# Kernel optimization log

Hardware: AMD Instinct MI355X
Metric: run time of the kernel (lower is better)

The kernel has to match this reference:

```python
import jax, jax.numpy as jnp
import numpy as np

SEQ_LEN = 8
NUM_HEADS = 8
LN_EPS = 1e-5
GN_EPS = 64e-5  # GroupNorm eps = head_dim * 1e-5 (RWKV7 convention, head_dim=64)


def layer_norm(x, w, b):
    mu = x.mean(-1, keepdims=True)
    var = ((x - mu) ** 2).mean(-1, keepdims=True)
    return (x - mu) / jnp.sqrt(var + LN_EPS) * w + b


def token_shift(x):
    # delta = shift(x) - x; shift prepends one zero token along time
    return jnp.pad(x, ((0, 0), (1, 0), (0, 0)))[:, :-1] - x


def group_norm(x, w, b, H):
    B, T, C = x.shape
    xh = x.reshape(B, T, H, C // H)
    mu = xh.mean(-1, keepdims=True)
    var = ((xh - mu) ** 2).mean(-1, keepdims=True)
    return ((xh - mu) / jnp.sqrt(var + GN_EPS)).reshape(B, T, C) * w + b


def rwkv7_scan(r, w, k, v, a, b, H):
    # Generalized delta-rule recurrence (RWKV7):
    #   S_t = S_{t-1} * diag(exp(-exp(w_t))) + (S_{t-1} a_t) b_t^T + v_t k_t^T
    #   o_t = S_t r_t
    B, T, C = r.shape
    N = C // H

    def tm(x):  # [B,T,C] -> [T,B,H,N] (time-major for scan)
        return x.reshape(B, T, H, N).transpose(1, 0, 2, 3)

    decay = jnp.exp(-jnp.exp(tm(w)))
    rs, ks, vs, as_, bs = tm(r), tm(k), tm(v), tm(a), tm(b)

    def step(S, inp):
        rt, dt, kt, vt, at, bt = inp  # each [B,H,N]
        sa = jnp.einsum('bhij,bhj->bhi', S, at)
        S = (S * dt[:, :, None, :]
             + sa[..., None] * bt[:, :, None, :]
             + vt[..., None] * kt[:, :, None, :])
        return S, jnp.einsum('bhij,bhj->bhi', S, rt)

    S0 = jnp.zeros((B, H, N, N), r.dtype)
    _, out = jax.lax.scan(step, S0, (rs, decay, ks, vs, as_, bs))
    return out.transpose(1, 0, 2, 3).reshape(B, T, C)


def _forward(image_tensor, pos_emb, xm, w0, w1, w2, a0, a1, a2, v0, v1, v2,
             g1, g2, kkp, kap, rkp, Wr, Wk, Wv, Wo, lnx_w, lnx_b,
             ln1_w, ln1_b, ln2_w, ln2_b, fxk, Wkey, Wval, lnf_w, lnf_b):
    EB, C, ih, iw = image_tensor.shape
    B = EB // SEQ_LEN
    H = NUM_HEADS
    x = image_tensor.transpose(0, 2, 3, 1).reshape(EB, ih * iw, C)
    x = (x + pos_emb).reshape(B, SEQ_LEN * ih * iw, C)  # [B, T, C]
    L = Wr.shape[0]
    v_first = None
    for l in range(L):
        # ---- time mix (RWKV7 attention) ----
        h = layer_norm(x, ln1_w[l], ln1_b[l])
        Bh, T, _ = h.shape
        dx = token_shift(h)
        xr, xw, xk, xv, xa, xg = [h + dx * xm[l, i] for i in range(6)]
        r = xr @ Wr[l]
        w = -jax.nn.softplus(-(w0[l] + jnp.tanh(xw @ w1[l]) @ w2[l])) - 0.5
        k = xk @ Wk[l]
        v = xv @ Wv[l]
        if v_first is None:
            v_first = v
        else:
            v = v + (v_first - v) * jax.nn.sigmoid(v0[l] + (xv @ v1[l]) @ v2[l])
        a = jax.nn.sigmoid(a0[l] + (xa @ a1[l]) @ a2[l])  # in-context lr
        g = jax.nn.sigmoid(xg @ g1[l]) @ g2[l]
        kk = (k * kkp[l]).reshape(Bh, T, H, -1)
        kk = kk / jnp.maximum(jnp.linalg.norm(kk, axis=-1, keepdims=True), 1e-12)
        kk = kk.reshape(Bh, T, C)
        k = k * (1.0 + (a - 1.0) * kap[l])
        o = rwkv7_scan(r, w, k, v, -kk, kk * a, H)
        o = group_norm(o, lnx_w[l], lnx_b[l], H)
        r4, k4, v4 = (t.reshape(Bh, T, H, -1) for t in (r, k, v))
        o = o + ((r4 * k4 * rkp[l]).sum(-1, keepdims=True) * v4).reshape(Bh, T, C)
        x = x + (o * g) @ Wo[l]
        # ---- channel mix (squared-ReLU FFN) ----
        h = layer_norm(x, ln2_w[l], ln2_b[l])
        kf = h + token_shift(h) * fxk[l]
        x = x + jnp.square(jax.nn.relu(kf @ Wkey[l])) @ Wval[l]
    x = layer_norm(x, lnf_w, lnf_b)
    return x.reshape(EB, ih, iw, C).transpose(0, 3, 1, 2)


def setup_inputs() -> dict:
    key = jax.random.key(0)
    ks = jax.random.split(key, 24)
    L, C, H = 8, 512, 8
    DW, DA, DV, DG, FF = 64, 64, 32, 128, 2048
    EB, IV, IW = 32, 8, 16
    FS = IV * IW

    def n(k, shape, s=0.02):
        return jax.random.normal(k, shape, jnp.float32) * s

    return dict(
        image_tensor=jax.random.normal(ks[0], (EB, C, IV, IW), jnp.float32),
        pos_emb=n(ks[1], (1, FS, C)),
        xm=jax.random.uniform(ks[2], (L, 6, C), jnp.float32),
        w0=n(ks[3], (L, C), 0.5) - 0.5,
        w1=n(ks[4], (L, C, DW), 0.02), w2=n(ks[5], (L, DW, C), 0.1),
        a0=jnp.zeros((L, C), jnp.float32),
        a1=n(ks[6], (L, C, DA)), a2=n(ks[7], (L, DA, C), 0.1),
        v0=jnp.ones((L, C), jnp.float32),
        v1=n(ks[8], (L, C, DV)), v2=n(ks[9], (L, DV, C), 0.1),
        g1=n(ks[10], (L, C, DG)), g2=n(ks[11], (L, DG, C), 0.1),
        kkp=jnp.full((L, C), 0.85, jnp.float32),
        kap=jnp.ones((L, C), jnp.float32),
        rkp=n(ks[12], (L, H, C // H), 0.3),
        Wr=n(ks[13], (L, C, C)), Wk=n(ks[14], (L, C, C)),
        Wv=n(ks[15], (L, C, C)), Wo=n(ks[16], (L, C, C)),
        lnx_w=jnp.ones((L, C), jnp.float32), lnx_b=jnp.zeros((L, C), jnp.float32),
        ln1_w=jnp.ones((L, C), jnp.float32), ln1_b=jnp.zeros((L, C), jnp.float32),
        ln2_w=jnp.ones((L, C), jnp.float32), ln2_b=jnp.zeros((L, C), jnp.float32),
        fxk=jax.random.uniform(ks[17], (L, C), jnp.float32),
        Wkey=n(ks[18], (L, C, FF)), Wval=n(ks[19], (L, FF, C)),
        lnf_w=jnp.ones((C,), jnp.float32), lnf_b=jnp.zeros((C,), jnp.float32),
    )


def reference(image_tensor, pos_emb, xm, w0, w1, w2, a0, a1, a2, v0, v1, v2,
              g1, g2, kkp, kap, rkp, Wr, Wk, Wv, Wo, lnx_w, lnx_b,
              ln1_w, ln1_b, ln2_w, ln2_b, fxk, Wkey, Wval, lnf_w, lnf_b):
    return _forward(image_tensor, pos_emb, xm, w0, w1, w2, a0, a1, a2, v0, v1,
                    v2, g1, g2, kkp, kap, rkp, Wr, Wk, Wv, Wo, lnx_w, lnx_b,
                    ln1_w, ln1_b, ln2_w, ln2_b, fxk, Wkey, Wval, lnf_w, lnf_b)
```

## Files before the change

kernel.cpp:

```cpp
#include <hip/hip_runtime.h>
#include <hip/hip_bf16.h>
#include <math.h>


#define NTOK 4096
#define CDIM 512
#define TT   1024
#define LC   64
#define NCH  16
#define TB   8

#define BM 128
#define BK 32

enum { EPI_NONE=0, EPI_TANH, EPI_SIG, EPI_DECAY, EPI_SIGB, EPI_VMIX, EPI_RELU2, EPI_ADD };

typedef short bf16x8 __attribute__((ext_vector_type(8)));
typedef float f32x4 __attribute__((ext_vector_type(4)));
typedef unsigned short ushort_t;

__device__ __forceinline__ float wsum64(float v) {
#pragma unroll
  for (int s = 1; s < 64; s <<= 1) v += __shfl_xor(v, s);
  return v;
}
__device__ __forceinline__ float gsum8(float v) {
  v += __shfl_xor(v, 1); v += __shfl_xor(v, 2); v += __shfl_xor(v, 4);
  return v;
}
__device__ __forceinline__ float sigm(float z) { return 1.f / (1.f + expf(-z)); }
__device__ __forceinline__ ushort_t f2bf(float x) {
  return __builtin_bit_cast(unsigned short, __float2bfloat16(x));
}
__device__ __forceinline__ void glds16(const void* g, void* l) {
  __builtin_amdgcn_global_load_lds(
      (const __attribute__((address_space(1))) void*)g,
      (__attribute__((address_space(3))) void*)l, 16, 0, 0);
}

struct Seg {
  const ushort_t* A; const ushort_t* B; void* C;
  const float* bias; const float* e1;
  int N; int K; int epi; int obf;
};
struct Segs4 { Seg s[4]; };

template<int BNt>
__global__ __launch_bounds__(256) void ggemm_k(Segs4 segs) {
  const Seg sg = segs.s[blockIdx.z];
  if (sg.epi < 0) return;
  constexpr int NCHK = 8 + BNt / 16;
  constexpr int LPW  = NCHK / 4;
  constexpr int WNF  = BNt / 32;
  __shared__ ushort_t As[3][BM * BK];
  __shared__ ushort_t Bs[3][BNt * BK];
  const ushort_t* __restrict__ A = sg.A;
  const ushort_t* __restrict__ B = sg.B;
  const int N = sg.N, K = sg.K;
  const int tid = threadIdx.x;
  const int wave = tid >> 6, lane = tid & 63;
  const int m0 = blockIdx.x * BM, n0 = blockIdx.y * BNt;
  const int wm = (wave >> 1) << 6, wn = (wave & 1) * (BNt / 2);

  f32x4 zero = {0.f, 0.f, 0.f, 0.f};
  f32x4 acc[4][WNF];
#pragma unroll
  for (int i = 0; i < 4; ++i)
#pragma unroll
    for (int j = 0; j < WNF; ++j) acc[i][j] = zero;

  const int crow = lane >> 2;
  const int soff = (((lane & 3) ^ (crow & 3)) << 3);
  const ushort_t* gptr[LPW];
  ushort_t* lbase[LPW];
  int lstr[LPW];
#pragma unroll
  for (int i = 0; i < LPW; ++i) {
    const int c = wave + 4 * i;
    if (c < 8) {
      gptr[i] = A + (size_t)(m0 + c * 16 + crow) * K + soff;
      lbase[i] = &As[0][c * 512 + lane * 8];
      lstr[i] = BM * BK;
    } else {
      gptr[i] = B + (size_t)(n0 + (c - 8) * 16 + crow) * K + soff;
      lbase[i] = &Bs[0][(c - 8) * 512 + lane * 8];
      lstr[i] = BNt * BK;
    }
  }

#define STAGE(bf_, k0_)                                        \
  { _Pragma("unroll") for (int i = 0; i < LPW; ++i)            \
      glds16(gptr[i] + (k0_), lbase[i] + (bf_) * lstr[i]); }

  const int rA = wm + (lane & 15);
  const int rB = wn + (lane & 15);
  const int kb = (((lane >> 4) ^ (lane & 3)) << 3);

#define COMPUTE(bf_)                                                          \
  {                                                                           \
    bf16x8 av[4], bvv[WNF];                                                   \
    _Pragma("unroll") for (int f = 0; f < 4; ++f)                             \
      av[f] = *(const bf16x8*)(&As[bf_][(rA + f * 16) * 32 + kb]);            \
    _Pragma("unroll") for (int f = 0; f < WNF; ++f)                           \
      bvv[f] = *(const bf16x8*)(&Bs[bf_][(rB + f * 16) * 32 + kb]);           \
    _Pragma("unroll") for (int i = 0; i < 4; ++i)                             \
      _Pragma("unroll") for (int j = 0; j < WNF; ++j)                         \
        acc[i][j] = __builtin_amdgcn_mfma_f32_16x16x32_bf16(av[i], bvv[j],    \
                                                            acc[i][j], 0, 0, 0); \
  }

  const int nk = K / BK;
  STAGE(0, 0);
  if (nk > 1) STAGE(1, BK);
  int bc = 0, bs = 2;
  for (int k = 0; k + 1 < nk; ++k) {
    asm volatile("s_waitcnt vmcnt(%0)" :: "i"(LPW) : "memory");
    __builtin_amdgcn_s_barrier();
    if (k + 2 < nk) {
      STAGE(bs, (k + 2) * BK);
      bs = (bs == 2) ? 0 : bs + 1;
    }
    COMPUTE(bc);
    bc = (bc == 2) ? 0 : bc + 1;
  }
  asm volatile("s_waitcnt vmcnt(0)" ::: "memory");
  __builtin_amdgcn_s_barrier();
  COMPUTE(bc);
#undef STAGE
#undef COMPUTE

  void* Cout = sg.C;
  const float* bias = sg.bias;
  const float* e1 = sg.e1;
  const int em = m0 + wm + ((lane >> 4) << 2);
  const int en = n0 + wn + (lane & 15);

#define EPI_STORE(EPI_, OBF_)                                                 \
  { _Pragma("unroll") for (int fi = 0; fi < 4; ++fi) {                        \
      _Pragma("unroll") for (int fj = 0; fj < WNF; ++fj) {                    \
        const int gn = en + fj * 16;                                          \
        if (gn < N) {                                                         \
          _Pragma("unroll") for (int rr = 0; rr < 4; ++rr) {                  \
            const int gm = em + fi * 16 + rr;                                 \
            const size_t idx = (size_t)gm * N + gn;                           \
            const float y = acc[fi][fj][rr];                                  \
            float outv;                                                       \
            if (EPI_ == EPI_NONE) { outv = y; }                               \
            else if (EPI_ == EPI_TANH) { outv = tanhf(y); }                   \
            else if (EPI_ == EPI_SIG) { outv = sigm(y); }                     \
            else if (EPI_ == EPI_DECAY) {                                     \
              const float z = bias[gn] + y;                                   \
              const float w = -log1pf(expf(-z)) - 0.5f;                       \
              outv = expf(-expf(w));                                          \
            } else if (EPI_ == EPI_SIGB) { outv = sigm(bias[gn] + y); }       \
            else if (EPI_ == EPI_VMIX) {                                      \
              const float vr = ((float*)Cout)[idx];                           \
              outv = vr + (e1[idx] - vr) * sigm(bias[gn] + y);                \
            } else if (EPI_ == EPI_RELU2) {                                   \
              const float t = fmaxf(y, 0.f); outv = t * t;                    \
            } else { outv = ((float*)Cout)[idx] + y; }                        \
            if (OBF_) ((ushort_t*)Cout)[idx] = f2bf(outv);                    \
            else      ((float*)Cout)[idx] = outv;                             \
          }                                                                   \
        }                                                                     \
      } } }

  switch (sg.epi) {
    case EPI_NONE:  if (sg.obf) EPI_STORE(EPI_NONE, 1) else EPI_STORE(EPI_NONE, 0); break;
    case EPI_TANH:  EPI_STORE(EPI_TANH, 1); break;
    case EPI_SIG:   EPI_STORE(EPI_SIG, 1); break;
    case EPI_DECAY: EPI_STORE(EPI_DECAY, 0); break;
    case EPI_SIGB:  EPI_STORE(EPI_SIGB, 0); break;
    case EPI_VMIX:  EPI_STORE(EPI_VMIX, 0); break;
    case EPI_RELU2: EPI_STORE(EPI_RELU2, 1); break;
    case EPI_ADD:   EPI_STORE(EPI_ADD, 0); break;
  }
#undef EPI_STORE
}

__global__ __launch_bounds__(256) void wprep_k(
    const float* __restrict__ in, ushort_t* __restrict__ out,
    int K, int N, int Npad)
{
  __shared__ float t[32][33];
  const int l = blockIdx.z;
  const int n0 = blockIdx.x * 32, k0 = blockIdx.y * 32;
  const int tx = threadIdx.x & 31, ty = threadIdx.x >> 5;
  const float* src = in + (size_t)l * K * N;
  ushort_t* dst = out + (size_t)l * Npad * K;
#pragma unroll
  for (int i = 0; i < 32; i += 8) {
    const int k = k0 + ty + i, n = n0 + tx;
    t[ty + i][tx] = (n < N) ? src[(size_t)k * N + n] : 0.f;
  }
  __syncthreads();
#pragma unroll
  for (int i = 0; i < 32; i += 8) {
    const int n = n0 + ty + i, k = k0 + tx;
    dst[(size_t)n * K + k] = f2bf(t[tx][ty + i]);
  }
}

__global__ __launch_bounds__(256) void lnmix6_k(
    const float* __restrict__ x, const float* __restrict__ w,
    const float* __restrict__ b, const float* __restrict__ xml,
    ushort_t* __restrict__ xr, ushort_t* __restrict__ xw,
    ushort_t* __restrict__ xk, ushort_t* __restrict__ xv,
    ushort_t* __restrict__ xa, ushort_t* __restrict__ xg)
{
  const int m = blockIdx.x * 4 + (threadIdx.x >> 6);
  const int lane = threadIdx.x & 63;
  const int c0 = lane << 3;
  const size_t idx = (size_t)m * CDIM + c0;
  const bool first = ((m & (TT - 1)) == 0);
  float v[8], p[8];
  *(float4*)&v[0] = *(const float4*)&x[idx];
  *(float4*)&v[4] = *(const float4*)&x[idx + 4];
  if (first) {
#pragma unroll
    for (int j = 0; j < 8; ++j) p[j] = 0.f;
  } else {
    *(float4*)&p[0] = *(const float4*)&x[idx - CDIM];
    *(float4*)&p[4] = *(const float4*)&x[idx - CDIM + 4];
  }
  float s = 0.f, sp = 0.f;
#pragma unroll
  for (int j = 0; j < 8; ++j) { s += v[j]; sp += p[j]; }
  s = wsum64(s); sp = wsum64(sp);
  const float mu = s * (1.f / 512.f), mup = sp * (1.f / 512.f);
  float q = 0.f, qp = 0.f;
#pragma unroll
  for (int j = 0; j < 8; ++j) {
    const float d1 = v[j] - mu, d2 = p[j] - mup;
    q += d1 * d1; qp += d2 * d2;
  }
  q = wsum64(q); qp = wsum64(qp);
  const float is = rsqrtf(q * (1.f / 512.f) + 1e-5f);
  const float isp = rsqrtf(qp * (1.f / 512.f) + 1e-5f);
  float wc[8], bc[8];
  *(float4*)&wc[0] = *(const float4*)&w[c0]; *(float4*)&wc[4] = *(const float4*)&w[c0 + 4];
  *(float4*)&bc[0] = *(const float4*)&b[c0]; *(float4*)&bc[4] = *(const float4*)&b[c0 + 4];
  float hv[8], dx[8];
#pragma unroll
  for (int j = 0; j < 8; ++j) {
    hv[j] = (v[j] - mu) * is * wc[j] + bc[j];
    const float hp = first ? 0.f : (p[j] - mup) * isp * wc[j] + bc[j];
    dx[j] = hp - hv[j];
  }
  ushort_t* outs[6] = {xr, xw, xk, xv, xa, xg};
#pragma unroll
  for (int o = 0; o < 6; ++o) {
    float mc[8];
    *(float4*)&mc[0] = *(const float4*)&xml[o * CDIM + c0];
    *(float4*)&mc[4] = *(const float4*)&xml[o * CDIM + c0 + 4];
    bf16x8 pk;
#pragma unroll
    for (int j = 0; j < 8; ++j) pk[j] = (short)f2bf(fmaf(dx[j], mc[j], hv[j]));
    *(bf16x8*)&outs[o][idx] = pk;
  }
}

__global__ __launch_bounds__(256) void lnmix1_k(
    const float* __restrict__ x, const float* __restrict__ w,
    const float* __restrict__ b, const float* __restrict__ coef,
    ushort_t* __restrict__ kf)
{
  const int m = blockIdx.x * 4 + (threadIdx.x >> 6);
  const int lane = threadIdx.x & 63;
  const int c0 = lane << 3;
  const size_t idx = (size_t)m * CDIM + c0;
  const bool first = ((m & (TT - 1)) == 0);
  float v[8], p[8];
  *(float4*)&v[0] = *(const float4*)&x[idx];
  *(float4*)&v[4] = *(const float4*)&x[idx + 4];
  if (first) {
#pragma unroll
    for (int j = 0; j < 8; ++j) p[j] = 0.f;
  } else {
    *(float4*)&p[0] = *(const float4*)&x[idx - CDIM];
    *(float4*)&p[4] = *(const float4*)&x[idx - CDIM + 4];
  }
  float s = 0.f, sp = 0.f;
#pragma unroll
  for (int j = 0; j < 8; ++j) { s += v[j]; sp += p[j]; }
  s = wsum64(s); sp = wsum64(sp);
  const float mu = s * (1.f / 512.f), mup = sp * (1.f / 512.f);
  float q = 0.f, qp = 0.f;
#pragma unroll
  for (int j = 0; j < 8; ++j) {
    const float d1 = v[j] - mu, d2 = p[j] - mup;
    q += d1 * d1; qp += d2 * d2;
  }
  q = wsum64(q); qp = wsum64(qp);
  const float is = rsqrtf(q * (1.f / 512.f) + 1e-5f);
  const float isp = rsqrtf(qp * (1.f / 512.f) + 1e-5f);
  bf16x8 pk;
#pragma unroll
  for (int j = 0; j < 8; ++j) {
    const float wc = w[c0 + j], bc = b[c0 + j];
    const float hv = (v[j] - mu) * is * wc + bc;
    const float hp = first ? 0.f : (p[j] - mup) * isp * wc + bc;
    pk[j] = (short)f2bf(fmaf(hp - hv, coef[c0 + j], hv));
  }
  *(bf16x8*)&kf[idx] = pk;
}

__global__ __launch_bounds__(256) void prep_k(
    float* __restrict__ k, const float* __restrict__ a,
    const float* __restrict__ kkp, const float* __restrict__ kap,
    float* __restrict__ aa, float* __restrict__ bb)
{
  const int m = blockIdx.x * 4 + (threadIdx.x >> 6);
  const int lane = threadIdx.x & 63;
  const int c0 = lane << 3;
  const size_t idx = (size_t)m * CDIM + c0;
  float kv[8], av[8], kp[8], ka[8];
  *(float4*)&kv[0] = *(const float4*)&k[idx];     *(float4*)&kv[4] = *(const float4*)&k[idx + 4];
  *(float4*)&av[0] = *(const float4*)&a[idx];     *(float4*)&av[4] = *(const float4*)&a[idx + 4];
  *(float4*)&kp[0] = *(const float4*)&kkp[c0];    *(float4*)&kp[4] = *(const float4*)&kkp[c0 + 4];
  *(float4*)&ka[0] = *(const float4*)&kap[c0];    *(float4*)&ka[4] = *(const float4*)&kap[c0 + 4];
  float kk[8], ss = 0.f;
#pragma unroll
  for (int j = 0; j < 8; ++j) { kk[j] = kv[j] * kp[j]; ss += kk[j] * kk[j]; }
  ss = gsum8(ss);
  const float rden = 1.f / fmaxf(sqrtf(ss), 1e-12f);
  float oaa[8], obb[8], okk[8];
#pragma unroll
  for (int j = 0; j < 8; ++j) {
    const float kkn = kk[j] * rden;
    oaa[j] = -kkn;
    obb[j] = kkn * av[j];
    okk[j] = kv[j] * (1.f + (av[j] - 1.f) * ka[j]);
  }
  *(float4*)&aa[idx] = *(float4*)&oaa[0]; *(float4*)&aa[idx + 4] = *(float4*)&oaa[4];
  *(float4*)&bb[idx] = *(float4*)&obb[0]; *(float4*)&bb[idx + 4] = *(float4*)&obb[4];
  *(float4*)&k[idx]  = *(float4*)&okk[0]; *(float4*)&k[idx + 4]  = *(float4*)&okk[4];
}

__global__ __launch_bounds__(256) void post_k(
    const float* __restrict__ o, const float* __restrict__ r,
    const float* __restrict__ k, const float* __restrict__ v,
    const float* __restrict__ g, const float* __restrict__ gw,
    const float* __restrict__ gb, const float* __restrict__ rkp,
    ushort_t* __restrict__ og)
{
  const int m = blockIdx.x * 4 + (threadIdx.x >> 6);
  const int lane = threadIdx.x & 63;
  const int c0 = lane << 3;
  const size_t idx = (size_t)m * CDIM + c0;
  float ov[8], rv[8], kv[8], vv[8], gv[8], rp[8];
  *(float4*)&ov[0] = *(const float4*)&o[idx];   *(float4*)&ov[4] = *(const float4*)&o[idx + 4];
  *(float4*)&rv[0] = *(const float4*)&r[idx];   *(float4*)&rv[4] = *(const float4*)&r[idx + 4];
  *(float4*)&kv[0] = *(const float4*)&k[idx];   *(float4*)&kv[4] = *(const float4*)&k[idx + 4];
  *(float4*)&vv[0] = *(const float4*)&v[idx];   *(float4*)&vv[4] = *(const float4*)&v[idx + 4];
  *(float4*)&gv[0] = *(const float4*)&g[idx];   *(float4*)&gv[4] = *(const float4*)&g[idx + 4];
  *(float4*)&rp[0] = *(const float4*)&rkp[c0];  *(float4*)&rp[4] = *(const float4*)&rkp[c0 + 4];
  float s = 0.f, dot = 0.f;
#pragma unroll
  for (int j = 0; j < 8; ++j) { s += ov[j]; dot += rv[j] * kv[j] * rp[j]; }
  s = gsum8(s); dot = gsum8(dot);
  const float mu = s * (1.f / 64.f);
  float q = 0.f;
#pragma unroll
  for (int j = 0; j < 8; ++j) { const float d = ov[j] - mu; q += d * d; }
  q = gsum8(q);
  const float is = rsqrtf(q * (1.f / 64.f) + 64e-5f);
  bf16x8 pk;
#pragma unroll
  for (int j = 0; j < 8; ++j) {
    const float gn = (ov[j] - mu) * is * gw[c0 + j] + gb[c0 + j];
    pk[j] = (short)f2bf((gn + dot * vv[j]) * gv[j]);
  }
  *(bf16x8*)&og[idx] = pk;
}

__global__ __launch_bounds__(512) void ln_final_k(
    const float* __restrict__ x, const float* __restrict__ w,
    const float* __restrict__ b, float* __restrict__ out)
{
  const int m = blockIdx.x, c = threadIdx.x;
  const size_t idx = (size_t)m * CDIM + c;
  const float v = x[idx];
  __shared__ float red[8], red2[8];
  float s = wsum64(v);
  if ((c & 63) == 0) red[c >> 6] = s;
  __syncthreads();
  float tot = 0.f;
#pragma unroll
  for (int u = 0; u < 8; ++u) tot += red[u];
  const float mu = tot * (1.f / 512.f);
  const float dv = v - mu;
  float s2 = wsum64(dv * dv);
  if ((c & 63) == 0) red2[c >> 6] = s2;
  __syncthreads();
  float vt = 0.f;
#pragma unroll
  for (int u = 0; u < 8; ++u) vt += red2[u];
  const float y = dv * rsqrtf(vt * (1.f / 512.f) + 1e-5f) * w[c] + b[c];
  const int bidx = m >> 10, t = m & 1023;
  const int p = t & 127, eb = bidx * 8 + (t >> 7);
  out[((size_t)eb * CDIM + c) * 128 + p] = y;
}

__global__ __launch_bounds__(512) void build_x_k(
    const float* __restrict__ img, const float* __restrict__ pos,
    float* __restrict__ x)
{
  const int m = blockIdx.x, c = threadIdx.x;
  const int bidx = m >> 10, t = m & 1023;
  const int p = t & 127, eb = bidx * 8 + (t >> 7);
  x[(size_t)m * CDIM + c] =
      img[((size_t)eb * CDIM + c) * 128 + p] + pos[(size_t)p * CDIM + c];
}

__global__ __launch_bounds__(256) void scan1_k(
    const float* __restrict__ d, const float* __restrict__ k,
    const float* __restrict__ v, const float* __restrict__ aa,
    const float* __restrict__ bb,
    float* __restrict__ P, float* __restrict__ Q)
{
  const int ch = blockIdx.x, bh = blockIdx.y;
  const int b = bh >> 3, hh = bh & 7;
  const int tid = threadIdx.x;
  const int i = tid >> 2, j0 = (tid & 3) << 4;
  float S[16], Pr[16];
#pragma unroll
  for (int u = 0; u < 16; ++u) { S[u] = 0.f; Pr[u] = (j0 + u == i) ? 1.f : 0.f; }

  __shared__ float sbuf[3][5 * TB * 64];
  const size_t base = (size_t)b * TT * CDIM + (size_t)ch * LC * CDIM + hh * 64;
  const float* srcs[5] = {d, k, v, aa, bb};
  const int f0 = tid, f1 = tid + 256, f2 = tid + 512;
  const float* gp0 = srcs[f0 >> 7] + base + (size_t)((f0 >> 4) & 7) * CDIM + ((f0 & 15) << 2);
  const float* gp1 = srcs[f1 >> 7] + base + (size_t)((f1 >> 4) & 7) * CDIM + ((f1 & 15) << 2);
  const float* gp2 = (tid < 128)
      ? srcs[f2 >> 7] + base + (size_t)((f2 >> 4) & 7) * CDIM + ((f2 & 15) << 2)
      : srcs[0];

#define STAGE1(bf_, goff_)                                     \
  {                                                            \
    glds16(gp0 + (goff_), &sbuf[bf_][f0 << 2]);                \
    glds16(gp1 + (goff_), &sbuf[bf_][f1 << 2]);                \
    if (tid < 128) glds16(gp2 + (goff_), &sbuf[bf_][f2 << 2]); \
  }

#define CGRP1(bf_)                                                              \
  {                                                                             \
    const float* sb0 = sbuf[bf_];                                               \
    _Pragma("unroll") for (int tt = 0; tt < TB; ++tt) {                         \
      const float* sd  = sb0 + 0 * TB * 64 + tt * 64;                           \
      const float* sk  = sb0 + 1 * TB * 64 + tt * 64;                           \
      const float* sv  = sb0 + 2 * TB * 64 + tt * 64;                           \
      const float* sa  = sb0 + 3 * TB * 64 + tt * 64;                           \
      const float* sbv = sb0 + 4 * TB * 64 + tt * 64;                           \
      float ps = 0.f, pp = 0.f;                                                 \
      _Pragma("unroll") for (int jj = 0; jj < 16; ++jj) {                       \
        ps = fmaf(S[jj],  sa[j0 + jj], ps);                                     \
        pp = fmaf(Pr[jj], sa[j0 + jj], pp);                                     \
      }                                                                         \
      ps += __shfl_xor(ps, 1); ps += __shfl_xor(ps, 2);                         \
      pp += __shfl_xor(pp, 1); pp += __shfl_xor(pp, 2);                         \
      const float vi = sv[i];                                                   \
      _Pragma("unroll") for (int jj = 0; jj < 16; ++jj) {                       \
        S[jj]  = fmaf(S[jj],  sd[j0 + jj], fmaf(ps, sbv[j0 + jj], vi * sk[j0 + jj])); \
        Pr[jj] = fmaf(Pr[jj], sd[j0 + jj], pp * sbv[j0 + jj]);                  \
      }                                                                         \
    }                                                                           \
  }

  constexpr int NG = LC / TB;
  STAGE1(0, 0);
  STAGE1(1, (size_t)TB * CDIM);
  int bc = 0, bs = 2;
  for (int g = 0; g + 1 < NG; ++g) {
    if (tid < 128) { asm volatile("s_waitcnt vmcnt(3)" ::: "memory"); }
    else           { asm volatile("s_waitcnt vmcnt(2)" ::: "memory"); }
    __builtin_amdgcn_s_barrier();
    if (g + 2 < NG) {
      STAGE1(bs, (size_t)(g + 2) * TB * CDIM);
      bs = (bs == 2) ? 0 : bs + 1;
    }
    CGRP1(bc);
    bc = (bc == 2) ? 0 : bc + 1;
  }
  asm volatile("s_waitcnt vmcnt(0)" ::: "memory");
  __builtin_amdgcn_s_barrier();
  CGRP1(bc);
#undef STAGE1
#undef CGRP1

  const size_t ob = ((size_t)(bh * NCH + ch)) * 4096 + (size_t)i * 64 + j0;
#pragma unroll
  for (int u = 0; u < 4; ++u) {
    *(float4*)&Q[ob + 4 * u] = make_float4(S[4*u], S[4*u+1], S[4*u+2], S[4*u+3]);
    *(float4*)&P[ob + 4 * u] = make_float4(Pr[4*u], Pr[4*u+1], Pr[4*u+2], Pr[4*u+3]);
  }
}

__global__ __launch_bounds__(512) void scan2_k(
    const float* __restrict__ P, const float* __restrict__ Q,
    float* __restrict__ Sst)
{
  const int tid = threadIdx.x;
  const int f0 = tid << 2;
  const int r0 = tid >> 4;
  const int c0 = (tid & 15) << 2;
  __shared__ float sP[4096];
  __shared__ float sS[4096];
  float4 S0 = {0.f, 0.f, 0.f, 0.f}, S1 = {0.f, 0.f, 0.f, 0.f};
  const size_t cbase = (size_t)blockIdx.x * NCH * 4096;
  float4 pf0 = *(const float4*)&P[cbase + f0];
  float4 pf1 = *(const float4*)&P[cbase + f0 + 2048];

  for (int c = 0; c < NCH; ++c) {
    const size_t cb = cbase + (size_t)c * 4096;
    *(float4*)&Sst[cb + f0] = S0;
    *(float4*)&Sst[cb + f0 + 2048] = S1;
    __syncthreads();
    *(float4*)&sP[f0] = pf0;  *(float4*)&sP[f0 + 2048] = pf1;
    *(float4*)&sS[f0] = S0;   *(float4*)&sS[f0 + 2048] = S1;
    __syncthreads();
    if (c + 1 < NCH) {
      pf0 = *(const float4*)&P[cb + 4096 + f0];
      pf1 = *(const float4*)&P[cb + 4096 + f0 + 2048];
    }
    const float4 q0 = *(const float4*)&Q[cb + f0];
    const float4 q1 = *(const float4*)&Q[cb + f0 + 2048];

    float a00 = 0.f, a01 = 0.f, a02 = 0.f, a03 = 0.f;
    float a10 = 0.f, a11 = 0.f, a12 = 0.f, a13 = 0.f;
    const float* sS0 = &sS[r0 * 64];
    const float* sS1 = &sS[(r0 + 32) * 64];
#pragma unroll
    for (int mm = 0; mm < 64; ++mm) {
      const float4 p4 = *(const float4*)&sP[mm * 64 + c0];
      const float u0 = sS0[mm], u1 = sS1[mm];
      a00 = fmaf(u0, p4.x, a00); a01 = fmaf(u0, p4.y, a01);
      a02 = fmaf(u0, p4.z, a02); a03 = fmaf(u0, p4.w, a03);
      a10 = fmaf(u1, p4.x, a10); a11 = fmaf(u1, p4.y, a11);
      a12 = fmaf(u1, p4.z, a12); a13 = fmaf(u1, p4.w, a13);
    }
    S0.x = a00 + q0.x; S0.y = a01 + q0.y; S0.z = a02 + q0.z; S0.w = a03 + q0.w;
    S1.x = a10 + q1.x; S1.y = a11 + q1.y; S1.z = a12 + q1.z; S1.w = a13 + q1.w;
  }
}

__global__ __launch_bounds__(256) void scan3_k(
    const float* __restrict__ r, const float* __restrict__ d,
    const float* __restrict__ k, const float* __restrict__ v,
    const float* __restrict__ aa, const float* __restrict__ bb,
    const float* __restrict__ Sst, float* __restrict__ o)
{
  const int ch = blockIdx.x, bh = blockIdx.y;
  const int b = bh >> 3, hh = bh & 7;
  const int tid = threadIdx.x;
  const int i = tid >> 2, q = tid & 3, j0 = q << 4;
  float S[16];
  const size_t sb_ = ((size_t)(bh * NCH + ch)) * 4096 + (size_t)i * 64 + j0;
#pragma unroll
  for (int u = 0; u < 4; ++u) {
    const float4 s4 = *(const float4*)&Sst[sb_ + 4 * u];
    S[4*u] = s4.x; S[4*u+1] = s4.y; S[4*u+2] = s4.z; S[4*u+3] = s4.w;
  }

  __shared__ float sbuf[3][6 * TB * 64];
  const size_t base = (size_t)b * TT * CDIM + (size_t)ch * LC * CDIM + hh * 64;
  const float* srcs[6] = {r, d, k, v, aa, bb};
  const int f0 = tid, f1 = tid + 256, f2 = tid + 512;
  const float* gp0 = srcs[f0 >> 7] + base + (size_t)((f0 >> 4) & 7) * CDIM + ((f0 & 15) << 2);
  const float* gp1 = srcs[f1 >> 7] + base + (size_t)((f1 >> 4) & 7) * CDIM + ((f1 & 15) << 2);
  const float* gp2 = srcs[f2 >> 7] + base + (size_t)((f2 >> 4) & 7) * CDIM + ((f2 & 15) << 2);

#define STAGE3(bf_, goff_)                          \
  {                                                 \
    glds16(gp0 + (goff_), &sbuf[bf_][f0 << 2]);     \
    glds16(gp1 + (goff_), &sbuf[bf_][f1 << 2]);     \
    glds16(gp2 + (goff_), &sbuf[bf_][f2 << 2]);     \
  }

#define CGRP3(bf_, g_)                                                          \
  {                                                                             \
    const float* sb0 = sbuf[bf_];                                               \
    const size_t obase = base + (size_t)(g_) * TB * CDIM;                       \
    _Pragma("unroll") for (int tt = 0; tt < TB; ++tt) {                         \
      const float* sr  = sb0 + 0 * TB * 64 + tt * 64;                           \
      const float* sd  = sb0 + 1 * TB * 64 + tt * 64;                           \
      const float* sk  = sb0 + 2 * TB * 64 + tt * 64;                           \
      const float* sv  = sb0 + 3 * TB * 64 + tt * 64;                           \
      const float* sa  = sb0 + 4 * TB * 64 + tt * 64;                           \
      const float* sbv = sb0 + 5 * TB * 64 + tt * 64;                           \
      float ps = 0.f, ps1 = 0.f;                                                \
      _Pragma("unroll") for (int jj = 0; jj < 16; jj += 2) {                    \
        ps  = fmaf(S[jj],     sa[j0 + jj],     ps);                             \
        ps1 = fmaf(S[jj + 1], sa[j0 + jj + 1], ps1);                            \
      }                                                                         \
      ps += ps1;                                                                \
      ps += __shfl_xor(ps, 1); ps += __shfl_xor(ps, 2);                         \
      const float vi = sv[i];                                                   \
      float po = 0.f, po1 = 0.f;                                                \
      _Pragma("unroll") for (int jj = 0; jj < 16; jj += 2) {                    \
        float s0 = fmaf(S[jj],     sd[j0 + jj],     fmaf(ps, sbv[j0 + jj],     vi * sk[j0 + jj])); \
        float s1 = fmaf(S[jj + 1], sd[j0 + jj + 1], fmaf(ps, sbv[j0 + jj + 1], vi * sk[j0 + jj + 1])); \
        S[jj] = s0; S[jj + 1] = s1;                                             \
        po  = fmaf(s0, sr[j0 + jj],     po);                                    \
        po1 = fmaf(s1, sr[j0 + jj + 1], po1);                                   \
      }                                                                         \
      po += po1;                                                                \
      po += __shfl_xor(po, 1); po += __shfl_xor(po, 2);                         \
      if (q == 0) o[obase + (size_t)tt * CDIM + i] = po;                        \
    }                                                                           \
  }

  constexpr int NG = LC / TB;
  STAGE3(0, 0);
  STAGE3(1, (size_t)TB * CDIM);
  int bc = 0, bs = 2;
  for (int g = 0; g + 1 < NG; ++g) {
    asm volatile("s_waitcnt vmcnt(3)" ::: "memory");
    __builtin_amdgcn_s_barrier();
    if (g + 2 < NG) {
      STAGE3(bs, (size_t)(g + 2) * TB * CDIM);
      bs = (bs == 2) ? 0 : bs + 1;
    }
    CGRP3(bc, g);
    bc = (bc == 2) ? 0 : bc + 1;
  }
  asm volatile("s_waitcnt vmcnt(0)" ::: "memory");
  __builtin_amdgcn_s_barrier();
  CGRP3(bc, NG - 1);
#undef STAGE3
#undef CGRP3
}

extern "C" void kernel_launch(void* const* d_in, const int* in_sizes, int n_in,
                              void* d_out, int out_size, void* d_ws, size_t ws_size,
                              hipStream_t stream) {
  (void)in_sizes; (void)n_in; (void)out_size; (void)ws_size;
  const float* img  = (const float*)d_in[0];
  const float* pos  = (const float*)d_in[1];
  const float* xm   = (const float*)d_in[2];
  const float* w0   = (const float*)d_in[3];
  const float* w1   = (const float*)d_in[4];
  const float* w2   = (const float*)d_in[5];
  const float* a0   = (const float*)d_in[6];
  const float* a1   = (const float*)d_in[7];
  const float* a2   = (const float*)d_in[8];
  const float* v0   = (const float*)d_in[9];
  const float* v1   = (const float*)d_in[10];
  const float* v2   = (const float*)d_in[11];
  const float* g1   = (const float*)d_in[12];
  const float* g2   = (const float*)d_in[13];
  const float* kkp  = (const float*)d_in[14];
  const float* kap  = (const float*)d_in[15];
  const float* rkp  = (const float*)d_in[16];
  const float* Wr   = (const float*)d_in[17];
  const float* Wk   = (const float*)d_in[18];
  const float* Wv   = (const float*)d_in[19];
  const float* Wo   = (const float*)d_in[20];
  const float* lnxw = (const float*)d_in[21];
  const float* lnxb = (const float*)d_in[22];
  const float* ln1w = (const float*)d_in[23];
  const float* ln1b = (const float*)d_in[24];
  const float* ln2w = (const float*)d_in[25];
  const float* ln2b = (const float*)d_in[26];
  const float* fxk  = (const float*)d_in[27];
  const float* Wkey = (const float*)d_in[28];
  const float* Wval = (const float*)d_in[29];
  const float* lnfw = (const float*)d_in[30];
  const float* lnfb = (const float*)d_in[31];

  float* ws = (float*)d_ws;
  const size_t SZ = (size_t)NTOK * CDIM;
  float* x   = ws + 0 * SZ;
  float* r_  = ws + 2 * SZ;
  float* dec = ws + 3 * SZ;
  float* k_  = ws + 4 * SZ;
  float* v_  = ws + 5 * SZ;
  float* vf  = ws + 6 * SZ;
  float* a_  = ws + 7 * SZ;
  float* g_  = ws + 8 * SZ;
  float* aa  = ws + 9 * SZ;
  float* bb  = ws + 10 * SZ;
  float* o_  = ws + 11 * SZ;
  float* mixf = ws + 12 * SZ;
  ushort_t* xr = (ushort_t*)mixf;
  ushort_t* xw = xr + SZ;
  ushort_t* xk = xr + 2 * SZ;
  ushort_t* xv = xr + 3 * SZ;
  ushort_t* xa = xr + 4 * SZ;
  ushort_t* xg = xr + 5 * SZ;
  float* Pbuf = mixf;
  float* Qbuf = mixf + SZ;
  float* Sst  = mixf + 2 * SZ;
  ushort_t* tmpb = (ushort_t*)(ws + 15 * SZ);
  ushort_t* t0b = tmpb;
  ushort_t* t1b = tmpb + (size_t)NTOK * 64;
  ushort_t* t2b = tmpb + (size_t)NTOK * 128;
  ushort_t* t3b = tmpb + (size_t)NTOK * 160;
  ushort_t* tfb  = (ushort_t*)(ws + 15 * SZ + SZ / 2);
  ushort_t* ogb  = (ushort_t*)(ws + 17 * SZ + SZ / 2);
  ushort_t* wb   = (ushort_t*)(ws + 18 * SZ);

  const size_t oWr  = 0;
  const size_t oWk  = oWr  + (size_t)8 * 512 * 512;
  const size_t oWv  = oWk  + (size_t)8 * 512 * 512;
  const size_t oWo  = oWv  + (size_t)8 * 512 * 512;
  const size_t oW1  = oWo  + (size_t)8 * 512 * 512;
  const size_t oW2  = oW1  + (size_t)8 * 128 * 512;
  const size_t oA1  = oW2  + (size_t)8 * 512 * 64;
  const size_t oA2  = oA1  + (size_t)8 * 128 * 512;
  const size_t oV1  = oA2  + (size_t)8 * 512 * 64;
  const size_t oV2  = oV1  + (size_t)8 * 128 * 512;
  const size_t oG1  = oV2  + (size_t)8 * 512 * 32;
  const size_t oG2  = oG1  + (size_t)8 * 128 * 512;
  const size_t oKey = oG2  + (size_t)8 * 512 * 128;
  const size_t oVal = oKey + (size_t)8 * 2048 * 512;

#define WPREP(src, dst, K_, N_, NP_) \
  wprep_k<<<dim3((NP_) / 32, (K_) / 32, 8), 256, 0, stream>>>(src, dst, K_, N_, NP_)
  WPREP(Wr,   wb + oWr,  512, 512, 512);
  WPREP(Wk,   wb + oWk,  512, 512, 512);
  WPREP(Wv,   wb + oWv,  512, 512, 512);
  WPREP(Wo,   wb + oWo,  512, 512, 512);
  WPREP(w1,   wb + oW1,  512, 64,  128);
  WPREP(w2,   wb + oW2,  64,  512, 512);
  WPREP(a1,   wb + oA1,  512, 64,  128);
  WPREP(a2,   wb + oA2,  64,  512, 512);
  WPREP(v1,   wb + oV1,  512, 32,  128);
  WPREP(v2,   wb + oV2,  32,  512, 512);
  WPREP(g1,   wb + oG1,  512, 128, 128);
  WPREP(g2,   wb + oG2,  128, 512, 512);
  WPREP(Wkey, wb + oKey, 512, 2048, 2048);
  WPREP(Wval, wb + oVal, 2048, 512, 512);
#undef WPREP

  build_x_k<<<NTOK, 512, 0, stream>>>(img, pos, x);

  for (int l = 0; l < 8; ++l) {
    const size_t lc = (size_t)l * CDIM;
    const float* xml = xm + (size_t)l * 6 * CDIM;
    const ushort_t* bWr = wb + oWr + (size_t)l * 512 * 512;
    const ushort_t* bWk = wb + oWk + (size_t)l * 512 * 512;
    const ushort_t* bWv = wb + oWv + (size_t)l * 512 * 512;
    const ushort_t* bWo = wb + oWo + (size_t)l * 512 * 512;
    const ushort_t* bW1 = wb + oW1 + (size_t)l * 128 * 512;
    const ushort_t* bW2 = wb + oW2 + (size_t)l * 512 * 64;
    const ushort_t* bA1 = wb + oA1 + (size_t)l * 128 * 512;
    const ushort_t* bA2 = wb + oA2 + (size_t)l * 512 * 64;
    const ushort_t* bV1 = wb + oV1 + (size_t)l * 128 * 512;
    const ushort_t* bV2 = wb + oV2 + (size_t)l * 512 * 32;
    const ushort_t* bG1 = wb + oG1 + (size_t)l * 128 * 512;
    const ushort_t* bG2 = wb + oG2 + (size_t)l * 512 * 128;
    const ushort_t* bKy = wb + oKey + (size_t)l * 2048 * 512;
    const ushort_t* bVl = wb + oVal + (size_t)l * 512 * 2048;
    float* vdst = (l == 0) ? vf : v_;

    lnmix6_k<<<NTOK / 4, 256, 0, stream>>>(x, ln1w + lc, ln1b + lc, xml,
                                           xr, xw, xk, xv, xa, xg);
    Segs4 qkv;
    qkv.s[0] = {xr, bWr, r_,   0, 0, 512, 512, EPI_NONE, 0};
    qkv.s[1] = {xk, bWk, k_,   0, 0, 512, 512, EPI_NONE, 0};
    qkv.s[2] = {xv, bWv, vdst, 0, 0, 512, 512, EPI_NONE, 0};
    qkv.s[3] = {0, 0, 0, 0, 0, 0, 0, -1, 0};
    ggemm_k<64><<<dim3(NTOK / BM, 8, 3), 256, 0, stream>>>(qkv);

    Segs4 dn;
    dn.s[0] = {xw, bW1, t0b, 0, 0, 64,  512, EPI_TANH, 1};
    dn.s[1] = {xa, bA1, t1b, 0, 0, 64,  512, EPI_NONE, 1};
    dn.s[2] = {xv, bV1, t2b, 0, 0, 32,  512, EPI_NONE, 1};
    dn.s[3] = {xg, bG1, t3b, 0, 0, 128, 512, EPI_SIG,  1};
    ggemm_k<64><<<dim3(NTOK / BM, 2, 4), 256, 0, stream>>>(dn);

    Segs4 up;
    up.s[0] = {t0b, bW2, dec, w0 + lc, 0,  512, 64,  EPI_DECAY, 0};
    up.s[1] = {t1b, bA2, a_,  a0 + lc, 0,  512, 64,  EPI_SIGB,  0};
    up.s[2] = {t2b, bV2, v_,  v0 + lc, vf, 512, 32,  (l > 0) ? EPI_VMIX : -1, 0};
    up.s[3] = {t3b, bG2, g_,  0, 0,        512, 128, EPI_NONE,  0};
    ggemm_k<64><<<dim3(NTOK / BM, 8, 4), 256, 0, stream>>>(up);

    const float* vptr = (l == 0) ? vf : v_;
    prep_k<<<NTOK / 4, 256, 0, stream>>>(k_, a_, kkp + lc, kap + lc, aa, bb);
    scan1_k<<<dim3(NCH, 32), 256, 0, stream>>>(dec, k_, vptr, aa, bb, Pbuf, Qbuf);
    scan2_k<<<32, 512, 0, stream>>>(Pbuf, Qbuf, Sst);
    scan3_k<<<dim3(NCH, 32), 256, 0, stream>>>(r_, dec, k_, vptr, aa, bb, Sst, o_);
    post_k<<<NTOK / 4, 256, 0, stream>>>(o_, r_, k_, vptr, g_, lnxw + lc, lnxb + lc,
                                         rkp + lc, ogb);
    Segs4 wo;
    wo.s[0] = {ogb, bWo, x, 0, 0, 512, 512, EPI_ADD, 0};
    wo.s[1] = wo.s[2] = wo.s[3] = {0, 0, 0, 0, 0, 0, 0, -1, 0};
    ggemm_k<64><<<dim3(NTOK / BM, 8, 1), 256, 0, stream>>>(wo);

    lnmix1_k<<<NTOK / 4, 256, 0, stream>>>(x, ln2w + lc, ln2b + lc, fxk + lc, xr);
    Segs4 f1;
    f1.s[0] = {xr, bKy, tfb, 0, 0, 2048, 512, EPI_RELU2, 1};
    f1.s[1] = f1.s[2] = f1.s[3] = {0, 0, 0, 0, 0, 0, 0, -1, 0};
    ggemm_k<64><<<dim3(NTOK / BM, 32, 1), 256, 0, stream>>>(f1);
    Segs4 f2;
    f2.s[0] = {tfb, bVl, x, 0, 0, 512, 2048, EPI_ADD, 0};
    f2.s[1] = f2.s[2] = f2.s[3] = {0, 0, 0, 0, 0, 0, 0, -1, 0};
    ggemm_k<64><<<dim3(NTOK / BM, 8, 1), 256, 0, stream>>>(f2);
  }

  ln_final_k<<<NTOK, 512, 0, stream>>>(x, lnfw, lnfb, (float*)d_out);
}
```

Before: 2.250 ms.

## Remap scan threads to 4x4 state tiles with DPP row reductions

In the chunked scan kernels (scan1 and scan3), each thread now owns a 4x4 tile of the 64x64 state instead of 16 contiguous columns of one row. This lets each thread read the per-step vectors from LDS as float4 and reuse them across four rows, cutting scalar LDS traffic. Row reductions move from __shfl_xor to 16-lane DPP row-rotate sums. The cost is more reduction steps per thread (four rows, four DPP stages each), and only the cg==0 lanes write the output, now as float4.

Measured after the change: 2.182 ms. 3.0% less time.

```diff
diff --git a/kernel.cpp b/kernel.cpp
--- a/kernel.cpp
+++ b/kernel.cpp
@@ -27,6 +27,18 @@
 __device__ __forceinline__ float gsum8(float v) {
   v += __shfl_xor(v, 1); v += __shfl_xor(v, 2); v += __shfl_xor(v, 4);
   return v;
+}
+__device__ __forceinline__ float rowsum16(float x) {
+  int t;
+  t = __builtin_amdgcn_mov_dpp(__builtin_bit_cast(int, x), 0x128, 0xF, 0xF, true);
+  x += __builtin_bit_cast(float, t);
+  t = __builtin_amdgcn_mov_dpp(__builtin_bit_cast(int, x), 0x124, 0xF, 0xF, true);
+  x += __builtin_bit_cast(float, t);
+  t = __builtin_amdgcn_mov_dpp(__builtin_bit_cast(int, x), 0x122, 0xF, 0xF, true);
+  x += __builtin_bit_cast(float, t);
+  t = __builtin_amdgcn_mov_dpp(__builtin_bit_cast(int, x), 0x121, 0xF, 0xF, true);
+  x += __builtin_bit_cast(float, t);
+  return x;
 }
 __device__ __forceinline__ float sigm(float z) { return 1.f / (1.f + expf(-z)); }
 __device__ __forceinline__ ushort_t f2bf(float x) {
@@ -422,10 +434,16 @@
   const int ch = blockIdx.x, bh = blockIdx.y;
   const int b = bh >> 3, hh = bh & 7;
   const int tid = threadIdx.x;
-  const int i = tid >> 2, j0 = (tid & 3) << 4;
+  const int rg = tid >> 4, cg = tid & 15;
+  const int r0 = rg << 2, c0 = cg << 2;
   float S[16], Pr[16];
 #pragma unroll
-  for (int u = 0; u < 16; ++u) { S[u] = 0.f; Pr[u] = (j0 + u == i) ? 1.f : 0.f; }
+  for (int ri = 0; ri < 4; ++ri)
+#pragma unroll
+    for (int cj = 0; cj < 4; ++cj) {
+      S[ri * 4 + cj] = 0.f;
+      Pr[ri * 4 + cj] = (r0 + ri == c0 + cj) ? 1.f : 0.f;
+    }
 
   __shared__ float sbuf[3][5 * TB * 64];
   const size_t base = (size_t)b * TT * CDIM + (size_t)ch * LC * CDIM + hh * 64;
@@ -453,18 +471,33 @@
       const float* sv  = sb0 + 2 * TB * 64 + tt * 64;                           \
       const float* sa  = sb0 + 3 * TB * 64 + tt * 64;                           \
       const float* sbv = sb0 + 4 * TB * 64 + tt * 64;                           \
-      float ps = 0.f, pp = 0.f;                                                 \
-      _Pragma("unroll") for (int jj = 0; jj < 16; ++jj) {                       \
-        ps = fmaf(S[jj],  sa[j0 + jj], ps);                                     \
-        pp = fmaf(Pr[jj], sa[j0 + jj], pp);                                     \
+      const float4 a4 = *(const float4*)(sa + c0);                              \
+      const float4 d4 = *(const float4*)(sd + c0);                              \
+      const float4 k4 = *(const float4*)(sk + c0);                              \
+      const float4 b4 = *(const float4*)(sbv + c0);                             \
+      const float4 v4 = *(const float4*)(sv + r0);                              \
+      const float dd[4] = {d4.x, d4.y, d4.z, d4.w};                             \
+      const float ak[4] = {a4.x, a4.y, a4.z, a4.w};                             \
+      const float kc[4] = {k4.x, k4.y, k4.z, k4.w};                             \
+      const float bc2[4] = {b4.x, b4.y, b4.z, b4.w};                            \
+      const float vr[4] = {v4.x, v4.y, v4.z, v4.w};                             \
+      float ps[4], pp[4];                                                       \
+      _Pragma("unroll") for (int ri = 0; ri < 4; ++ri) {                        \
+        ps[ri] = fmaf(S[ri*4+0], ak[0], fmaf(S[ri*4+1], ak[1],                  \
+                 fmaf(S[ri*4+2], ak[2], S[ri*4+3] * ak[3])));                   \
+        pp[ri] = fmaf(Pr[ri*4+0], ak[0], fmaf(Pr[ri*4+1], ak[1],                \
+                 fmaf(Pr[ri*4+2], ak[2], Pr[ri*4+3] * ak[3])));                 \
       }                                                                         \
-      ps += __shfl_xor(ps, 1); ps += __shfl_xor(ps, 2);                         \
-      pp += __shfl_xor(pp, 1); pp += __shfl_xor(pp, 2);                         \
-      const float vi = sv[i];                                                   \
-      _Pragma("unroll") for (int jj = 0; jj < 16; ++jj) {                       \
-        S[jj]  = fmaf(S[jj],  sd[j0 + jj], fmaf(ps, sbv[j0 + jj], vi * sk[j0 + jj])); \
-        Pr[jj] = fmaf(Pr[jj], sd[j0 + jj], pp * sbv[j0 + jj]);                  \
+      _Pragma("unroll") for (int ri = 0; ri < 4; ++ri) {                        \
+        ps[ri] = rowsum16(ps[ri]);                                              \
+        pp[ri] = rowsum16(pp[ri]);                                              \
       }                                                                         \
+      _Pragma("unroll") for (int ri = 0; ri < 4; ++ri)                          \
+        _Pragma("unroll") for (int cj = 0; cj < 4; ++cj) {                      \
+          S[ri*4+cj]  = fmaf(S[ri*4+cj], dd[cj],                                \
+                        fmaf(ps[ri], bc2[cj], vr[ri] * kc[cj]));                \
+          Pr[ri*4+cj] = fmaf(Pr[ri*4+cj], dd[cj], pp[ri] * bc2[cj]);            \
+        }                                                                       \
     }                                                                           \
   }
 
@@ -489,11 +522,11 @@
 #undef STAGE1
 #undef CGRP1
 
-  const size_t ob = ((size_t)(bh * NCH + ch)) * 4096 + (size_t)i * 64 + j0;
-#pragma unroll
-  for (int u = 0; u < 4; ++u) {
-    *(float4*)&Q[ob + 4 * u] = make_float4(S[4*u], S[4*u+1], S[4*u+2], S[4*u+3]);
-    *(float4*)&P[ob + 4 * u] = make_float4(Pr[4*u], Pr[4*u+1], Pr[4*u+2], Pr[4*u+3]);
+  const size_t ob = ((size_t)(bh * NCH + ch)) * 4096 + (size_t)r0 * 64 + c0;
+#pragma unroll
+  for (int ri = 0; ri < 4; ++ri) {
+    *(float4*)&Q[ob + ri * 64] = make_float4(S[ri*4+0], S[ri*4+1], S[ri*4+2], S[ri*4+3]);
+    *(float4*)&P[ob + ri * 64] = make_float4(Pr[ri*4+0], Pr[ri*4+1], Pr[ri*4+2], Pr[ri*4+3]);
   }
 }
 
@@ -554,13 +587,14 @@
   const int ch = blockIdx.x, bh = blockIdx.y;
   const int b = bh >> 3, hh = bh & 7;
   const int tid = threadIdx.x;
-  const int i = tid >> 2, q = tid & 3, j0 = q << 4;
+  const int rg = tid >> 4, cg = tid & 15;
+  const int r0 = rg << 2, c0 = cg << 2;
   float S[16];
-  const size_t sb_ = ((size_t)(bh * NCH + ch)) * 4096 + (size_t)i * 64 + j0;
-#pragma unroll
-  for (int u = 0; u < 4; ++u) {
-    const float4 s4 = *(const float4*)&Sst[sb_ + 4 * u];
-    S[4*u] = s4.x; S[4*u+1] = s4.y; S[4*u+2] = s4.z; S[4*u+3] = s4.w;
+  const size_t sb_ = ((size_t)(bh * NCH + ch)) * 4096 + (size_t)r0 * 64 + c0;
+#pragma unroll
+  for (int ri = 0; ri < 4; ++ri) {
+    const float4 s4 = *(const float4*)&Sst[sb_ + ri * 64];
+    S[ri*4+0] = s4.x; S[ri*4+1] = s4.y; S[ri*4+2] = s4.z; S[ri*4+3] = s4.w;
   }
 
   __shared__ float sbuf[3][6 * TB * 64];
@@ -589,25 +623,41 @@
       const float* sv  = sb0 + 3 * TB * 64 + tt * 64;                           \
       const float* sa  = sb0 + 4 * TB * 64 + tt * 64;                           \
       const float* sbv = sb0 + 5 * TB * 64 + tt * 64;                           \
-      float ps = 0.f, ps1 = 0.f;                                                \
-      _Pragma("unroll") for (int jj = 0; jj < 16; jj += 2) {                    \
-        ps  = fmaf(S[jj],     sa[j0 + jj],     ps);                             \
-        ps1 = fmaf(S[jj + 1], sa[j0 + jj + 1], ps1);                            \
+      const float4 a4 = *(const float4*)(sa + c0);                              \
+      const float4 d4 = *(const float4*)(sd + c0);                              \
+      const float4 k4 = *(const float4*)(sk + c0);                              \
+      const float4 b4 = *(const float4*)(sbv + c0);                             \
+      const float4 r4 = *(const float4*)(sr + c0);                              \
+      const float4 v4 = *(const float4*)(sv + r0);                              \
+      const float dd[4] = {d4.x, d4.y, d4.z, d4.w};                             \
+      const float ak[4] = {a4.x, a4.y, a4.z, a4.w};                             \
+      const float kc[4] = {k4.x, k4.y, k4.z, k4.w};                             \
+      const float bc2[4] = {b4.x, b4.y, b4.z, b4.w};                            \
+      const float rr[4] = {r4.x, r4.y, r4.z, r4.w};                             \
+      const float vr[4] = {v4.x, v4.y, v4.z, v4.w};                             \
+      float ps[4];                                                              \
+      _Pragma("unroll") for (int ri = 0; ri < 4; ++ri)                          \
+        ps[ri] = fmaf(S[ri*4+0], ak[0], fmaf(S[ri*4+1], ak[1],                  \
+                 fmaf(S[ri*4+2], ak[2], S[ri*4+3] * ak[3])));                   \
+      _Pragma("unroll") for (int ri = 0; ri < 4; ++ri)                          \
+        ps[ri] = rowsum16(ps[ri]);                                              \
+      float po[4];                                                              \
+      _Pragma("unroll") for (int ri = 0; ri < 4; ++ri) {                        \
+        float acc_ = 0.f;                                                       \
+        _Pragma("unroll") for (int cj = 0; cj < 4; ++cj) {                      \
+          const float sn = fmaf(S[ri*4+cj], dd[cj],                             \
+                           fmaf(ps[ri], bc2[cj], vr[ri] * kc[cj]));             \
+          S[ri*4+cj] = sn;                                                      \
+          acc_ = fmaf(sn, rr[cj], acc_);                                        \
+        }                                                                       \
+        po[ri] = acc_;                                                          \
       }                                                                         \
-      ps += ps1;                                                                \
-      ps += __shfl_xor(ps, 1); ps += __shfl_xor(ps, 2);                         \
-      const float vi = sv[i];                                                   \
-      float po = 0.f, po1 = 0.f;                                                \
-      _Pragma("unroll") for (int jj = 0; jj < 16; jj += 2) {                    \
-        float s0 = fmaf(S[jj],     sd[j0 + jj],     fmaf(ps, sbv[j0 + jj],     vi * sk[j0 + jj])); \
-        float s1 = fmaf(S[jj + 1], sd[j0 + jj + 1], fmaf(ps, sbv[j0 + jj + 1], vi * sk[j0 + jj + 1])); \
-        S[jj] = s0; S[jj + 1] = s1;                                             \
-        po  = fmaf(s0, sr[j0 + jj],     po);                                    \
-        po1 = fmaf(s1, sr[j0 + jj + 1], po1);                                   \
+      _Pragma("unroll") for (int ri = 0; ri < 4; ++ri)                          \
+        po[ri] = rowsum16(po[ri]);                                              \
+      if (cg == 0) {                                                            \
+        float4 po4 = make_float4(po[0], po[1], po[2], po[3]);                   \
+        *(float4*)&o[obase + (size_t)tt * CDIM + r0] = po4;                     \
       }                                                                         \
-      po += po1;                                                                \
-      po += __shfl_xor(po, 1); po += __shfl_xor(po, 2);                         \
-      if (q == 0) o[obase + (size_t)tt * CDIM + i] = po;                        \
     }                                                                           \
   }
 
```
